# Kernel tuning notes

Measured on AMD Instinct MI355X. Metric: run time of the kernel, lower is better.

## Reference

```python
import jax, jax.numpy as jnp
import numpy as np

N_NODES = 50000
N_EDGES = 800000
F_IN = 128
F_OUT = 128


def setup_inputs() -> dict:
    key = jax.random.key(0)
    k1, k2, k3, k4 = jax.random.split(key, 4)
    x = jax.random.normal(k1, (N_NODES, F_IN), dtype=jnp.float32)
    edge_index = jax.random.randint(k2, (2, N_EDGES), 0, N_NODES, dtype=jnp.int64)
    edge_weight = jax.random.uniform(k3, (N_EDGES,), dtype=jnp.float32)
    # GCNConv linear weight (applied as x @ W) and bias
    W = jax.random.normal(k4, (F_IN, F_OUT), dtype=jnp.float32) / np.sqrt(F_IN)
    b = jnp.zeros((F_OUT,), dtype=jnp.float32)
    return {"x": x, "edge_index": edge_index, "edge_weight": edge_weight, "W": W, "b": b}


def reference(x, edge_index, edge_weight, W, b):
    """Single GCNConv forward (PyG semantics: normalize=True, add_self_loops=True).

    out[i] = sum_{(j->i) in E'} norm_ji * (x[j] @ W) + b
    where E' = E + self loops (weight 1), norm = D^{-1/2} A D^{-1/2}.
    """
    n = x.shape[0]
    # add self loops with weight 1.0
    loops = jnp.arange(n, dtype=edge_index.dtype)
    row = jnp.concatenate([edge_index[0], loops])  # source nodes
    col = jnp.concatenate([edge_index[1], loops])  # target nodes
    ew = jnp.concatenate([edge_weight, jnp.ones((n,), dtype=edge_weight.dtype)])
    # symmetric degree normalization (degree computed at targets, as in PyG gcn_norm)
    deg = jax.ops.segment_sum(ew, col, num_segments=n)
    dinv = jnp.where(deg > 0, jax.lax.rsqrt(deg), 0.0)
    norm = dinv[row] * ew * dinv[col]  # [E+N]
    # linear transform then gather-scale-scatter aggregation
    h = x @ W  # [N, F_OUT]
    msgs = norm[:, None] * h[row]  # [E+N, F_OUT]
    out = jax.ops.segment_sum(msgs, col, num_segments=n) + b
    return out
```

## Files before the change

kernel.cpp:

```cpp
#include <hip/hip_runtime.h>


#define F 128
#define MAXOVF 4096
#define SHIFT 7
#define RNG 128
#define NBMAX 512
#define SA_BS 1024
#define SA_EPB 4096

typedef __attribute__((ext_vector_type(8))) short bf16x8;
typedef __attribute__((ext_vector_type(4))) float f32x4;

__device__ __forceinline__ unsigned bf16rne(float f) {
    unsigned u = __float_as_uint(f);
    return (u + 0x7fffu + ((u >> 16) & 1u)) >> 16;
}
__device__ __forceinline__ float bflo(unsigned u) { return __uint_as_float(u << 16); }
__device__ __forceinline__ float bfhi(unsigned u) { return __uint_as_float(u & 0xffff0000u); }

__global__ __launch_bounds__(1024) void sortA_k(
        const int* __restrict__ row, const int* __restrict__ col,
        const float* __restrict__ ew, const float* __restrict__ x,
        const float* __restrict__ W,
        unsigned* __restrict__ gcnt,
        unsigned long long* __restrict__ stage,
        unsigned* __restrict__ ovf_w, int* __restrict__ ovf, int* __restrict__ ovfc,
        uint4* __restrict__ xb4, unsigned short* __restrict__ Wt,
        int E, int NB, int capb, int SAB, int XB4, long ng8) {
    int tid = threadIdx.x;
    int blk = blockIdx.x;
    if (blk >= SAB) {
        if (blk < SAB + XB4) {
            long i = (long)(blk - SAB) * 1024 + tid;
            if (i < ng8) {
                const float4* x4 = (const float4*)x;
                float4 a = x4[2 * i], c = x4[2 * i + 1];
                uint4 o;
                o.x = bf16rne(a.x) | (bf16rne(a.y) << 16);
                o.y = bf16rne(a.z) | (bf16rne(a.w) << 16);
                o.z = bf16rne(c.x) | (bf16rne(c.y) << 16);
                o.w = bf16rne(c.z) | (bf16rne(c.w) << 16);
                xb4[i] = o;
            }
        } else {
            int idx = (blk - SAB - XB4) * 1024 + tid;
            if (idx < F * F) {
                int k = idx >> 7, nn = idx & 127;
                Wt[nn * F + k] = (unsigned short)bf16rne(W[idx]);
            }
        }
        return;
    }
    __shared__ unsigned hist[NBMAX], sc[NBMAX], rbase[NBMAX], ravail[NBMAX];
    __shared__ unsigned long long stg[SA_EPB];
    unsigned xcc;
    asm volatile("s_getreg_b32 %0, hwreg(HW_REG_XCC_ID, 0, 4)" : "=s"(xcc));
    xcc &= 7u;
    long e0 = (long)blk * SA_EPB;
    for (int i = tid; i < NBMAX; i += SA_BS) hist[i] = 0;
    __syncthreads();
    unsigned long long pk[4];
    int bk[4]; unsigned rk[4];
    #pragma unroll
    for (int k = 0; k < 4; ++k) {
        long e = e0 + k * SA_BS + tid;
        bk[k] = -1;
        if (e < E) {
            int c = col[e], r = row[e];
            float w = ew[e];
            unsigned wq = __float2uint_rn(w * 32768.0f);
            if (wq > 32767u) wq = 32767u;
            pk[k] = ((unsigned long long)(unsigned)c << 32) |
                    ((unsigned long long)(unsigned)r << 15) | wq;
            bk[k] = c >> SHIFT;
            rk[k] = atomicAdd(&hist[bk[k]], 1u);
        }
    }
    __syncthreads();
    if (tid < NBMAX) sc[tid] = hist[tid];
    __syncthreads();
    for (int d = 1; d < NBMAX; d <<= 1) {
        unsigned v = 0;
        if (tid < NBMAX && tid >= d) v = sc[tid - d];
        __syncthreads();
        if (tid < NBMAX) sc[tid] += v;
        __syncthreads();
    }
    if (tid < NB) {
        unsigned cnt = hist[tid], bs = 0, av = 0;
        if (cnt > 0) {
            bs = atomicAdd(&gcnt[xcc * NBMAX + tid], cnt);
            av = (bs < (unsigned)capb) ? ((unsigned)capb - bs) : 0u;
        }
        rbase[tid] = bs;
        ravail[tid] = av;
    }
    __syncthreads();
    #pragma unroll
    for (int k = 0; k < 4; ++k)
        if (bk[k] >= 0) stg[sc[bk[k]] - hist[bk[k]] + rk[k]] = pk[k];
    __syncthreads();
    int tot = (int)sc[NBMAX - 1];
    for (int i = tid; i < tot; i += SA_BS) {
        int lo = 0, hi = NB - 1;
        while (lo < hi) {
            int mid = (lo + hi + 1) >> 1;
            if (sc[mid] - hist[mid] <= (unsigned)i) lo = mid; else hi = mid - 1;
        }
        unsigned j = (unsigned)i - (sc[lo] - hist[lo]);
        unsigned long long v = stg[i];
        if (j < ravail[lo]) {
            stage[((size_t)lo * 8 + xcc) * capb + rbase[lo] + j] = v;
        } else {
            int c = (int)(v >> 32);
            int r = (int)((v >> 15) & 0x1FFFFu);
            unsigned wq = (unsigned)(v & 0x7FFFu);
            atomicAdd(&ovf_w[c], wq);
            int p = atomicAdd(ovfc, 1);
            if (p < MAXOVF) {
                ovf[3 * p] = r; ovf[3 * p + 1] = c; ovf[3 * p + 2] = (int)wq;
            }
        }
    }
}

__global__ __launch_bounds__(1024) void sortB_k(
        const unsigned long long* __restrict__ stage,
        const unsigned* __restrict__ gcnt, const unsigned* __restrict__ ovf_w,
        unsigned* __restrict__ eout, int* __restrict__ offA, int* __restrict__ cntA,
        float* __restrict__ dinv, int n, int capb) {
    __shared__ unsigned cnt[RNG], wsum[RNG], scn[RNG], bex[RNG];
    __shared__ unsigned rpre[9];
    int tid = threadIdx.x;
    int b = blockIdx.x;
    int node0 = b << SHIFT;
    int nodes = n - node0; if (nodes > RNG) nodes = RNG; if (nodes < 0) nodes = 0;
    if (tid < RNG) { cnt[tid] = 0; wsum[tid] = 0; }
    if (tid == 0) {
        unsigned acc = 0; rpre[0] = 0;
        #pragma unroll
        for (int xr = 0; xr < 8; ++xr) {
            unsigned m = gcnt[xr * NBMAX + b]; if (m > (unsigned)capb) m = capb;
            acc += m; rpre[xr + 1] = acc;
        }
    }
    __syncthreads();
    int T = (int)rpre[8];
    unsigned ent[8]; unsigned short noa[8], rka[8];
    int myc = 0;
    for (int i = tid; i < T; i += 1024) {
        int xr = 0;
        while (rpre[xr + 1] <= (unsigned)i) ++xr;
        unsigned j = (unsigned)i - rpre[xr];
        unsigned long long v = stage[((size_t)b * 8 + xr) * capb + j];
        int no = (int)(v >> 32) - node0;
        unsigned wq = (unsigned)(v & 0x7FFFu);
        unsigned rk = atomicAdd(&cnt[no], 1u);
        atomicAdd(&wsum[no], wq);
        ent[myc] = (unsigned)((((v >> 15) & 0x1FFFFu) << 15) | wq);
        noa[myc] = (unsigned short)no; rka[myc] = (unsigned short)rk;
        ++myc;
    }
    __syncthreads();
    if (tid < RNG) scn[tid] = cnt[tid];
    __syncthreads();
    for (int d = 1; d < RNG; d <<= 1) {
        unsigned v = 0;
        if (tid < RNG && tid >= d) v = scn[tid - d];
        __syncthreads();
        if (tid < RNG) scn[tid] += v;
        __syncthreads();
    }
    if (tid < RNG) bex[tid] = scn[tid] - cnt[tid];
    __syncthreads();
    if (tid < nodes) {
        int node = node0 + tid;
        float deg = (float)(wsum[tid] + ovf_w[node]) * (1.0f / 32768.0f) + 1.0f;
        dinv[node] = rsqrtf(deg);
        offA[node] = b * (capb * 8) + (int)bex[tid];
        cntA[node] = (int)cnt[tid];
    }
    unsigned base = (unsigned)(b * (capb * 8));
    for (int k = 0; k < myc; ++k)
        eout[base + bex[noa[k]] + rka[k]] = ent[k];
}

__global__ __launch_bounds__(256) void aggregate_k(
        const uint4* __restrict__ xb4, const float* __restrict__ dinv,
        const int* __restrict__ offA, const int* __restrict__ cntA,
        const unsigned* __restrict__ eout,
        const int* __restrict__ ovf, const int* __restrict__ ovfc,
        uint4* __restrict__ yb4, int n) {
    int lane = threadIdx.x & 63, wv = threadIdx.x >> 6;
    int g = lane >> 4, l = lane & 15;
    int i = blockIdx.x * 16 + wv * 4 + g;
    if (i >= n) return;
    float di = dinv[i];
    uint4 xs = xb4[(size_t)i * 16 + l];
    float a0 = di * bflo(xs.x), a1 = di * bfhi(xs.x);
    float a2 = di * bflo(xs.y), a3 = di * bfhi(xs.y);
    float a4 = di * bflo(xs.z), a5 = di * bfhi(xs.z);
    float a6 = di * bflo(xs.w), a7 = di * bfhi(xs.w);
    int cnt = cntA[i], off = offA[i];
    for (int bb = 0; bb < cnt; bb += 32) {
        int e0 = bb + 2 * l;
        unsigned m0 = (e0     < cnt) ? eout[off + e0]     : 0u;
        unsigned m1 = (e0 + 1 < cnt) ? eout[off + e0 + 1] : 0u;
        int sv0 = (int)(m0 >> 15), sv1 = (int)(m1 >> 15);
        float wk0 = (float)(m0 & 0x7FFFu) * (1.0f / 32768.0f) * dinv[sv0];
        float wk1 = (float)(m1 & 0x7FFFu) * (1.0f / 32768.0f) * dinv[sv1];
        int cb = cnt - bb; if (cb > 32) cb = 32;
        for (int j0 = 0; j0 < cb; j0 += 8) {
            int base = g * 16 + (j0 >> 1);
            int   s0 = __shfl(sv0, base),     s1 = __shfl(sv1, base);
            int   s2 = __shfl(sv0, base + 1), s3 = __shfl(sv1, base + 1);
            int   s4 = __shfl(sv0, base + 2), s5 = __shfl(sv1, base + 2);
            int   s6 = __shfl(sv0, base + 3), s7 = __shfl(sv1, base + 3);
            float w0 = __shfl(wk0, base),     w1 = __shfl(wk1, base);
            float w2 = __shfl(wk0, base + 1), w3 = __shfl(wk1, base + 1);
            float w4 = __shfl(wk0, base + 2), w5 = __shfl(wk1, base + 2);
            float w6 = __shfl(wk0, base + 3), w7 = __shfl(wk1, base + 3);
            uint4 u0 = xb4[(size_t)s0 * 16 + l];
            uint4 u1 = xb4[(size_t)s1 * 16 + l];
            uint4 u2 = xb4[(size_t)s2 * 16 + l];
            uint4 u3 = xb4[(size_t)s3 * 16 + l];
            uint4 u4 = xb4[(size_t)s4 * 16 + l];
            uint4 u5 = xb4[(size_t)s5 * 16 + l];
            uint4 u6 = xb4[(size_t)s6 * 16 + l];
            uint4 u7 = xb4[(size_t)s7 * 16 + l];
            a0 += w0 * bflo(u0.x) + w1 * bflo(u1.x) + w2 * bflo(u2.x) + w3 * bflo(u3.x)
                + w4 * bflo(u4.x) + w5 * bflo(u5.x) + w6 * bflo(u6.x) + w7 * bflo(u7.x);
            a1 += w0 * bfhi(u0.x) + w1 * bfhi(u1.x) + w2 * bfhi(u2.x) + w3 * bfhi(u3.x)
                + w4 * bfhi(u4.x) + w5 * bfhi(u5.x) + w6 * bfhi(u6.x) + w7 * bfhi(u7.x);
            a2 += w0 * bflo(u0.y) + w1 * bflo(u1.y) + w2 * bflo(u2.y) + w3 * bflo(u3.y)
                + w4 * bflo(u4.y) + w5 * bflo(u5.y) + w6 * bflo(u6.y) + w7 * bflo(u7.y);
            a3 += w0 * bfhi(u0.y) + w1 * bfhi(u1.y) + w2 * bfhi(u2.y) + w3 * bfhi(u3.y)
                + w4 * bfhi(u4.y) + w5 * bfhi(u5.y) + w6 * bfhi(u6.y) + w7 * bfhi(u7.y);
            a4 += w0 * bflo(u0.z) + w1 * bflo(u1.z) + w2 * bflo(u2.z) + w3 * bflo(u3.z)
                + w4 * bflo(u4.z) + w5 * bflo(u5.z) + w6 * bflo(u6.z) + w7 * bflo(u7.z);
            a5 += w0 * bfhi(u0.z) + w1 * bfhi(u1.z) + w2 * bfhi(u2.z) + w3 * bfhi(u3.z)
                + w4 * bfhi(u4.z) + w5 * bfhi(u5.z) + w6 * bfhi(u6.z) + w7 * bfhi(u7.z);
            a6 += w0 * bflo(u0.w) + w1 * bflo(u1.w) + w2 * bflo(u2.w) + w3 * bflo(u3.w)
                + w4 * bflo(u4.w) + w5 * bflo(u5.w) + w6 * bflo(u6.w) + w7 * bflo(u7.w);
            a7 += w0 * bfhi(u0.w) + w1 * bfhi(u1.w) + w2 * bfhi(u2.w) + w3 * bfhi(u3.w)
                + w4 * bfhi(u4.w) + w5 * bfhi(u5.w) + w6 * bfhi(u6.w) + w7 * bfhi(u7.w);
        }
    }
    int oc = *ovfc;
    if (oc > 0) {
        if (oc > MAXOVF) oc = MAXOVF;
        for (int k = 0; k < oc; ++k) {
            if (ovf[3 * k + 1] == i) {
                int sv = ovf[3 * k];
                float wk = (float)ovf[3 * k + 2] * (1.0f / 32768.0f) * dinv[sv];
                uint4 u = xb4[(size_t)sv * 16 + l];
                a0 += wk * bflo(u.x); a1 += wk * bfhi(u.x);
                a2 += wk * bflo(u.y); a3 += wk * bfhi(u.y);
                a4 += wk * bflo(u.z); a5 += wk * bfhi(u.z);
                a6 += wk * bflo(u.w); a7 += wk * bfhi(u.w);
            }
        }
    }
    a0 *= di; a1 *= di; a2 *= di; a3 *= di;
    a4 *= di; a5 *= di; a6 *= di; a7 *= di;
    uint4 o;
    o.x = bf16rne(a0) | (bf16rne(a1) << 16);
    o.y = bf16rne(a2) | (bf16rne(a3) << 16);
    o.z = bf16rne(a4) | (bf16rne(a5) << 16);
    o.w = bf16rne(a6) | (bf16rne(a7) << 16);
    yb4[(size_t)i * 16 + l] = o;
}

__global__ __launch_bounds__(256) void gemm_k(const unsigned short* __restrict__ yb,
        const unsigned short* __restrict__ Wt, const float* __restrict__ bias,
        float* __restrict__ out, int n) {
    __shared__ float cs[4][16 * 132];
    int tid = threadIdx.x;
    int w = tid >> 6, lane = tid & 63;
    int m = lane & 15, q = lane >> 4;
    int r0 = blockIdx.x * 64 + w * 16;
    int ar = r0 + m;
    if (ar >= n) ar = n - 1;
    const unsigned short* arow = yb + (size_t)ar * F + q * 8;

    f32x4 acc[8];
    #pragma unroll
    for (int t = 0; t < 8; ++t) acc[t] = (f32x4){0.f, 0.f, 0.f, 0.f};

    #pragma unroll
    for (int kk = 0; kk < 4; ++kk) {
        bf16x8 a = *(const bf16x8*)(arow + kk * 32);
        #pragma unroll
        for (int t = 0; t < 8; ++t) {
            bf16x8 bfr = *(const bf16x8*)(Wt + (size_t)(t * 16 + m) * F + kk * 32 + q * 8);
            acc[t] = __builtin_amdgcn_mfma_f32_16x16x32_bf16(a, bfr, acc[t], 0, 0, 0);
        }
    }

    float* csw = cs[w];
    #pragma unroll
    for (int t = 0; t < 8; ++t)
        #pragma unroll
        for (int v = 0; v < 4; ++v)
            csw[(q * 4 + v) * 132 + t * 16 + m] = acc[t][v];
    int cg = lane & 31;
    float4 bv4 = ((const float4*)bias)[cg];
    #pragma unroll
    for (int rp = 0; rp < 8; ++rp) {
        int rowl = rp * 2 + (lane >> 5);
        int rr = r0 + rowl;
        float4 v4 = *(float4*)&csw[rowl * 132 + cg * 4];
        v4.x += bv4.x; v4.y += bv4.y; v4.z += bv4.z; v4.w += bv4.w;
        if (rr < n) ((float4*)out)[(size_t)rr * 32 + cg] = v4;
    }
}

extern "C" void kernel_launch(void* const* d_in, const int* in_sizes, int n_in,
                              void* d_out, int out_size, void* d_ws, size_t ws_size,
                              hipStream_t stream) {
    const float* x  = (const float*)d_in[0];
    const int*   ei = (const int*)d_in[1];
    const float* ew = (const float*)d_in[2];
    const float* W  = (const float*)d_in[3];
    const float* b  = (const float*)d_in[4];
    float* out = (float*)d_out;

    int n = in_sizes[0] / F;
    int E = in_sizes[2];
    const int* row = ei;
    const int* col = ei + E;
    int NB = (n + RNG - 1) >> SHIFT;

    float* ws = (float*)d_ws;
    size_t o = 0;
    auto take = [&](size_t elems) { size_t r = o; o += (elems + 63) & ~63ull; return r; };
    size_t o_gcnt  = take(8 * NBMAX);
    size_t o_ovfc  = take(64);
    size_t o_ovfw  = take(n);
    size_t zero_end = o;
    size_t o_ovf   = take((size_t)MAXOVF * 3);
    size_t o_dinv  = take(n);
    size_t o_offA  = take(n);
    size_t o_cntA  = take(n);
    size_t o_wt    = take(F * F / 2);
    size_t o_xb    = take((size_t)n * (F / 2));
    size_t o_yb    = take((size_t)n * (F / 2));
    size_t units = ws_size / 4;
    size_t remain = (units > o + 128) ? (units - o - 128) : 0;
    int capb = (int)(remain / ((size_t)NB * 8 * 3));
    if (capb > 1024) capb = 1024;
    if (capb < 256)  capb = 256;
    size_t o_stage = take((size_t)NB * 8 * capb * 2);
    size_t o_eout  = take((size_t)NB * 8 * capb);
    (void)n_in; (void)out_size; (void)o_eout;

    unsigned* gcnt = (unsigned*)(ws + o_gcnt);
    int*      ovfc = (int*)(ws + o_ovfc);
    unsigned* ovfw = (unsigned*)(ws + o_ovfw);
    int*      ovf  = (int*)(ws + o_ovf);
    float*    dinv = ws + o_dinv;
    int*      offA = (int*)(ws + o_offA);
    int*      cntA = (int*)(ws + o_cntA);
    unsigned short* Wt = (unsigned short*)(ws + o_wt);
    unsigned* xb   = (unsigned*)(ws + o_xb);
    unsigned* yb   = (unsigned*)(ws + o_yb);
    unsigned long long* stage = (unsigned long long*)(ws + o_stage);
    unsigned* eout = (unsigned*)(ws + o_eout);

    hipMemsetAsync(d_ws, 0, zero_end * sizeof(float), stream);

    int SAB = (E + SA_EPB - 1) / SA_EPB;
    long ng8 = (long)n * (F / 8);
    int XB4 = (int)((ng8 + 1023) / 1024);
    int WB = (F * F + 1023) / 1024;

    sortA_k<<<SAB + XB4 + WB, SA_BS, 0, stream>>>(row, col, ew, x, W, gcnt, stage,
                                                  ovfw, ovf, ovfc, (uint4*)xb, Wt,
                                                  E, NB, capb, SAB, XB4, ng8);
    sortB_k<<<NB, SA_BS, 0, stream>>>(stage, gcnt, ovfw, eout, offA, cntA,
                                      dinv, n, capb);
    aggregate_k<<<(n + 15) / 16, 256, 0, stream>>>((const uint4*)xb, dinv, offA,
                                                   cntA, eout, ovf, ovfc,
                                                   (uint4*)yb, n);
    gemm_k<<<(n + 63) / 64, 256, 0, stream>>>((const unsigned short*)yb, Wt, b, out, n);
}
```

Before: 150.9 us.

## Fuse aggregation with bf16 MFMA GEMM and cache bucket ids in sort

Aggregation and the projection GEMM are merged into one kernel. Each 512-thread block aggregates 32 nodes into shared memory, then runs MFMA against the transposed weights and writes the output with bias added. This removes the bf16 intermediate buffer's global write and read plus one kernel launch. Separately, the sort pass stores each staged entry's bucket id in shared memory, replacing a per-element binary search over the prefix sums. In exchange, the extra shared memory and the launch-bounds hint may lower occupancy during the gather-heavy aggregation phase.

```diff
diff --git a/kernel.cpp b/kernel.cpp
--- a/kernel.cpp
+++ b/kernel.cpp
@@ -54,6 +54,7 @@
     }
     __shared__ unsigned hist[NBMAX], sc[NBMAX], rbase[NBMAX], ravail[NBMAX];
     __shared__ unsigned long long stg[SA_EPB];
+    __shared__ unsigned short bkid[SA_EPB];
     unsigned xcc;
     asm volatile("s_getreg_b32 %0, hwreg(HW_REG_XCC_ID, 0, 4)" : "=s"(xcc));
     xcc &= 7u;
@@ -99,15 +100,15 @@
     __syncthreads();
     #pragma unroll
     for (int k = 0; k < 4; ++k)
-        if (bk[k] >= 0) stg[sc[bk[k]] - hist[bk[k]] + rk[k]] = pk[k];
+        if (bk[k] >= 0) {
+            unsigned slot = sc[bk[k]] - hist[bk[k]] + rk[k];
+            stg[slot] = pk[k];
+            bkid[slot] = (unsigned short)bk[k];
+        }
     __syncthreads();
     int tot = (int)sc[NBMAX - 1];
     for (int i = tid; i < tot; i += SA_BS) {
-        int lo = 0, hi = NB - 1;
-        while (lo < hi) {
-            int mid = (lo + hi + 1) >> 1;
-            if (sc[mid] - hist[mid] <= (unsigned)i) lo = mid; else hi = mid - 1;
-        }
+        int lo = (int)bkid[i];
         unsigned j = (unsigned)i - (sc[lo] - hist[lo]);
         unsigned long long v = stg[i];
         if (j < ravail[lo]) {
@@ -186,133 +187,131 @@
         eout[base + bex[noa[k]] + rka[k]] = ent[k];
 }
 
-__global__ __launch_bounds__(256) void aggregate_k(
+__global__ __launch_bounds__(512, 6) void agg_gemm_k(
         const uint4* __restrict__ xb4, const float* __restrict__ dinv,
         const int* __restrict__ offA, const int* __restrict__ cntA,
         const unsigned* __restrict__ eout,
         const int* __restrict__ ovf, const int* __restrict__ ovfc,
-        uint4* __restrict__ yb4, int n) {
-    int lane = threadIdx.x & 63, wv = threadIdx.x >> 6;
-    int g = lane >> 4, l = lane & 15;
-    int i = blockIdx.x * 16 + wv * 4 + g;
-    if (i >= n) return;
-    float di = dinv[i];
-    uint4 xs = xb4[(size_t)i * 16 + l];
-    float a0 = di * bflo(xs.x), a1 = di * bfhi(xs.x);
-    float a2 = di * bflo(xs.y), a3 = di * bfhi(xs.y);
-    float a4 = di * bflo(xs.z), a5 = di * bfhi(xs.z);
-    float a6 = di * bflo(xs.w), a7 = di * bfhi(xs.w);
-    int cnt = cntA[i], off = offA[i];
-    for (int bb = 0; bb < cnt; bb += 32) {
-        int e0 = bb + 2 * l;
-        unsigned m0 = (e0     < cnt) ? eout[off + e0]     : 0u;
-        unsigned m1 = (e0 + 1 < cnt) ? eout[off + e0 + 1] : 0u;
-        int sv0 = (int)(m0 >> 15), sv1 = (int)(m1 >> 15);
-        float wk0 = (float)(m0 & 0x7FFFu) * (1.0f / 32768.0f) * dinv[sv0];
-        float wk1 = (float)(m1 & 0x7FFFu) * (1.0f / 32768.0f) * dinv[sv1];
-        int cb = cnt - bb; if (cb > 32) cb = 32;
-        for (int j0 = 0; j0 < cb; j0 += 8) {
-            int base = g * 16 + (j0 >> 1);
-            int   s0 = __shfl(sv0, base),     s1 = __shfl(sv1, base);
-            int   s2 = __shfl(sv0, base + 1), s3 = __shfl(sv1, base + 1);
-            int   s4 = __shfl(sv0, base + 2), s5 = __shfl(sv1, base + 2);
-            int   s6 = __shfl(sv0, base + 3), s7 = __shfl(sv1, base + 3);
-            float w0 = __shfl(wk0, base),     w1 = __shfl(wk1, base);
-            float w2 = __shfl(wk0, base + 1), w3 = __shfl(wk1, base + 1);
-            float w4 = __shfl(wk0, base + 2), w5 = __shfl(wk1, base + 2);
-            float w6 = __shfl(wk0, base + 3), w7 = __shfl(wk1, base + 3);
-            uint4 u0 = xb4[(size_t)s0 * 16 + l];
-            uint4 u1 = xb4[(size_t)s1 * 16 + l];
-            uint4 u2 = xb4[(size_t)s2 * 16 + l];
-            uint4 u3 = xb4[(size_t)s3 * 16 + l];
-            uint4 u4 = xb4[(size_t)s4 * 16 + l];
-            uint4 u5 = xb4[(size_t)s5 * 16 + l];
-            uint4 u6 = xb4[(size_t)s6 * 16 + l];
-            uint4 u7 = xb4[(size_t)s7 * 16 + l];
-            a0 += w0 * bflo(u0.x) + w1 * bflo(u1.x) + w2 * bflo(u2.x) + w3 * bflo(u3.x)
-                + w4 * bflo(u4.x) + w5 * bflo(u5.x) + w6 * bflo(u6.x) + w7 * bflo(u7.x);
-            a1 += w0 * bfhi(u0.x) + w1 * bfhi(u1.x) + w2 * bfhi(u2.x) + w3 * bfhi(u3.x)
-                + w4 * bfhi(u4.x) + w5 * bfhi(u5.x) + w6 * bfhi(u6.x) + w7 * bfhi(u7.x);
-            a2 += w0 * bflo(u0.y) + w1 * bflo(u1.y) + w2 * bflo(u2.y) + w3 * bflo(u3.y)
-                + w4 * bflo(u4.y) + w5 * bflo(u5.y) + w6 * bflo(u6.y) + w7 * bflo(u7.y);
-            a3 += w0 * bfhi(u0.y) + w1 * bfhi(u1.y) + w2 * bfhi(u2.y) + w3 * bfhi(u3.y)
-                + w4 * bfhi(u4.y) + w5 * bfhi(u5.y) + w6 * bfhi(u6.y) + w7 * bfhi(u7.y);
-            a4 += w0 * bflo(u0.z) + w1 * bflo(u1.z) + w2 * bflo(u2.z) + w3 * bflo(u3.z)
-                + w4 * bflo(u4.z) + w5 * bflo(u5.z) + w6 * bflo(u6.z) + w7 * bflo(u7.z);
-            a5 += w0 * bfhi(u0.z) + w1 * bfhi(u1.z) + w2 * bfhi(u2.z) + w3 * bfhi(u3.z)
-                + w4 * bfhi(u4.z) + w5 * bfhi(u5.z) + w6 * bfhi(u6.z) + w7 * bfhi(u7.z);
-            a6 += w0 * bflo(u0.w) + w1 * bflo(u1.w) + w2 * bflo(u2.w) + w3 * bflo(u3.w)
-                + w4 * bflo(u4.w) + w5 * bflo(u5.w) + w6 * bflo(u6.w) + w7 * bflo(u7.w);
-            a7 += w0 * bfhi(u0.w) + w1 * bfhi(u1.w) + w2 * bfhi(u2.w) + w3 * bfhi(u3.w)
-                + w4 * bfhi(u4.w) + w5 * bfhi(u5.w) + w6 * bfhi(u6.w) + w7 * bfhi(u7.w);
-        }
-    }
-    int oc = *ovfc;
-    if (oc > 0) {
-        if (oc > MAXOVF) oc = MAXOVF;
-        for (int k = 0; k < oc; ++k) {
-            if (ovf[3 * k + 1] == i) {
-                int sv = ovf[3 * k];
-                float wk = (float)ovf[3 * k + 2] * (1.0f / 32768.0f) * dinv[sv];
-                uint4 u = xb4[(size_t)sv * 16 + l];
-                a0 += wk * bflo(u.x); a1 += wk * bfhi(u.x);
-                a2 += wk * bflo(u.y); a3 += wk * bfhi(u.y);
-                a4 += wk * bflo(u.z); a5 += wk * bfhi(u.z);
-                a6 += wk * bflo(u.w); a7 += wk * bfhi(u.w);
-            }
-        }
-    }
-    a0 *= di; a1 *= di; a2 *= di; a3 *= di;
-    a4 *= di; a5 *= di; a6 *= di; a7 *= di;
-    uint4 o;
-    o.x = bf16rne(a0) | (bf16rne(a1) << 16);
-    o.y = bf16rne(a2) | (bf16rne(a3) << 16);
-    o.z = bf16rne(a4) | (bf16rne(a5) << 16);
-    o.w = bf16rne(a6) | (bf16rne(a7) << 16);
-    yb4[(size_t)i * 16 + l] = o;
-}
-
-__global__ __launch_bounds__(256) void gemm_k(const unsigned short* __restrict__ yb,
         const unsigned short* __restrict__ Wt, const float* __restrict__ bias,
         float* __restrict__ out, int n) {
-    __shared__ float cs[4][16 * 132];
-    int tid = threadIdx.x;
-    int w = tid >> 6, lane = tid & 63;
-    int m = lane & 15, q = lane >> 4;
-    int r0 = blockIdx.x * 64 + w * 16;
-    int ar = r0 + m;
-    if (ar >= n) ar = n - 1;
-    const unsigned short* arow = yb + (size_t)ar * F + q * 8;
-
-    f32x4 acc[8];
-    #pragma unroll
-    for (int t = 0; t < 8; ++t) acc[t] = (f32x4){0.f, 0.f, 0.f, 0.f};
-
-    #pragma unroll
-    for (int kk = 0; kk < 4; ++kk) {
-        bf16x8 a = *(const bf16x8*)(arow + kk * 32);
+    __shared__ unsigned ys[32 * 68];
+    __shared__ float epi[8][2 * 320];
+    int wv = threadIdx.x >> 6, lane = threadIdx.x & 63;
+
+    {
+        int g = lane >> 4, l = lane & 15;
+        int nl = wv * 4 + g;
+        int i = blockIdx.x * 32 + nl;
+        if (i < n) {
+            float di = dinv[i];
+            uint4 xs = xb4[(size_t)i * 16 + l];
+            float a0 = di * bflo(xs.x), a1 = di * bfhi(xs.x);
+            float a2 = di * bflo(xs.y), a3 = di * bfhi(xs.y);
+            float a4 = di * bflo(xs.z), a5 = di * bfhi(xs.z);
+            float a6 = di * bflo(xs.w), a7 = di * bfhi(xs.w);
+            int cnt = cntA[i], off = offA[i];
+            for (int bb = 0; bb < cnt; bb += 32) {
+                int e0 = bb + 2 * l;
+                unsigned m0 = (e0     < cnt) ? eout[off + e0]     : 0u;
+                unsigned m1 = (e0 + 1 < cnt) ? eout[off + e0 + 1] : 0u;
+                int sv0 = (int)(m0 >> 15), sv1 = (int)(m1 >> 15);
+                float wk0 = (float)(m0 & 0x7FFFu) * (1.0f / 32768.0f) * dinv[sv0];
+                float wk1 = (float)(m1 & 0x7FFFu) * (1.0f / 32768.0f) * dinv[sv1];
+                int cb = cnt - bb; if (cb > 32) cb = 32;
+                for (int j0 = 0; j0 < cb; j0 += 8) {
+                    int base = g * 16 + (j0 >> 1);
+                    int   s0 = __shfl(sv0, base),     s1 = __shfl(sv1, base);
+                    int   s2 = __shfl(sv0, base + 1), s3 = __shfl(sv1, base + 1);
+                    int   s4 = __shfl(sv0, base + 2), s5 = __shfl(sv1, base + 2);
+                    int   s6 = __shfl(sv0, base + 3), s7 = __shfl(sv1, base + 3);
+                    float w0 = __shfl(wk0, base),     w1 = __shfl(wk1, base);
+                    float w2 = __shfl(wk0, base + 1), w3 = __shfl(wk1, base + 1);
+                    float w4 = __shfl(wk0, base + 2), w5 = __shfl(wk1, base + 2);
+                    float w6 = __shfl(wk0, base + 3), w7 = __shfl(wk1, base + 3);
+                    uint4 u0 = xb4[(size_t)s0 * 16 + l];
+                    uint4 u1 = xb4[(size_t)s1 * 16 + l];
+                    uint4 u2 = xb4[(size_t)s2 * 16 + l];
+                    uint4 u3 = xb4[(size_t)s3 * 16 + l];
+                    uint4 u4 = xb4[(size_t)s4 * 16 + l];
+                    uint4 u5 = xb4[(size_t)s5 * 16 + l];
+                    uint4 u6 = xb4[(size_t)s6 * 16 + l];
+                    uint4 u7 = xb4[(size_t)s7 * 16 + l];
+                    a0 += w0 * bflo(u0.x) + w1 * bflo(u1.x) + w2 * bflo(u2.x) + w3 * bflo(u3.x)
+                        + w4 * bflo(u4.x) + w5 * bflo(u5.x) + w6 * bflo(u6.x) + w7 * bflo(u7.x);
+                    a1 += w0 * bfhi(u0.x) + w1 * bfhi(u1.x) + w2 * bfhi(u2.x) + w3 * bfhi(u3.x)
+                        + w4 * bfhi(u4.x) + w5 * bfhi(u5.x) + w6 * bfhi(u6.x) + w7 * bfhi(u7.x);
+                    a2 += w0 * bflo(u0.y) + w1 * bflo(u1.y) + w2 * bflo(u2.y) + w3 * bflo(u3.y)
+                        + w4 * bflo(u4.y) + w5 * bflo(u5.y) + w6 * bflo(u6.y) + w7 * bflo(u7.y);
+                    a3 += w0 * bfhi(u0.y) + w1 * bfhi(u1.y) + w2 * bfhi(u2.y) + w3 * bfhi(u3.y)
+                        + w4 * bfhi(u4.y) + w5 * bfhi(u5.y) + w6 * bfhi(u6.y) + w7 * bfhi(u7.y);
+                    a4 += w0 * bflo(u0.z) + w1 * bflo(u1.z) + w2 * bflo(u2.z) + w3 * bflo(u3.z)
+                        + w4 * bflo(u4.z) + w5 * bflo(u5.z) + w6 * bflo(u6.z) + w7 * bflo(u7.z);
+                    a5 += w0 * bfhi(u0.z) + w1 * bfhi(u1.z) + w2 * bfhi(u2.z) + w3 * bfhi(u3.z)
+                        + w4 * bfhi(u4.z) + w5 * bfhi(u5.z) + w6 * bfhi(u6.z) + w7 * bfhi(u7.z);
+                    a6 += w0 * bflo(u0.w) + w1 * bflo(u1.w) + w2 * bflo(u2.w) + w3 * bflo(u3.w)
+                        + w4 * bflo(u4.w) + w5 * bflo(u5.w) + w6 * bflo(u6.w) + w7 * bflo(u7.w);
+                    a7 += w0 * bfhi(u0.w) + w1 * bfhi(u1.w) + w2 * bfhi(u2.w) + w3 * bfhi(u3.w)
+                        + w4 * bfhi(u4.w) + w5 * bfhi(u5.w) + w6 * bfhi(u6.w) + w7 * bfhi(u7.w);
+                }
+            }
+            int oc = *ovfc;
+            if (oc > 0) {
+                if (oc > MAXOVF) oc = MAXOVF;
+                for (int k = 0; k < oc; ++k) {
+                    if (ovf[3 * k + 1] == i) {
+                        int sv = ovf[3 * k];
+                        float wk = (float)ovf[3 * k + 2] * (1.0f / 32768.0f) * dinv[sv];
+                        uint4 u = xb4[(size_t)sv * 16 + l];
+                        a0 += wk * bflo(u.x); a1 += wk * bfhi(u.x);
+                        a2 += wk * bflo(u.y); a3 += wk * bfhi(u.y);
+                        a4 += wk * bflo(u.z); a5 += wk * bfhi(u.z);
+                        a6 += wk * bflo(u.w); a7 += wk * bfhi(u.w);
+                    }
+                }
+            }
+            a0 *= di; a1 *= di; a2 *= di; a3 *= di;
+            a4 *= di; a5 *= di; a6 *= di; a7 *= di;
+            uint4 o;
+            o.x = bf16rne(a0) | (bf16rne(a1) << 16);
+            o.y = bf16rne(a2) | (bf16rne(a3) << 16);
+            o.z = bf16rne(a4) | (bf16rne(a5) << 16);
+            o.w = bf16rne(a6) | (bf16rne(a7) << 16);
+            *(uint4*)&ys[nl * 68 + l * 4] = o;
+        }
+    }
+    __syncthreads();
+
+    {
+        int m = lane & 15, q = lane >> 4;
+        int rt = wv & 1;
+        int ct0 = wv >> 1;
+        int gr0 = blockIdx.x * 32 + rt * 16;
+        f32x4 acc0 = (f32x4){0.f, 0.f, 0.f, 0.f};
+        f32x4 acc1 = (f32x4){0.f, 0.f, 0.f, 0.f};
         #pragma unroll
-        for (int t = 0; t < 8; ++t) {
-            bf16x8 bfr = *(const bf16x8*)(Wt + (size_t)(t * 16 + m) * F + kk * 32 + q * 8);
-            acc[t] = __builtin_amdgcn_mfma_f32_16x16x32_bf16(a, bfr, acc[t], 0, 0, 0);
-        }
-    }
-
-    float* csw = cs[w];
-    #pragma unroll
-    for (int t = 0; t < 8; ++t)
+        for (int kk = 0; kk < 4; ++kk) {
+            bf16x8 a = *(const bf16x8*)&ys[(rt * 16 + m) * 68 + kk * 16 + q * 4];
+            bf16x8 b0 = *(const bf16x8*)(Wt + (size_t)(ct0 * 16 + m) * F + kk * 32 + q * 8);
+            bf16x8 b1 = *(const bf16x8*)(Wt + (size_t)((ct0 + 4) * 16 + m) * F + kk * 32 + q * 8);
+            acc0 = __builtin_amdgcn_mfma_f32_16x16x32_bf16(a, b0, acc0, 0, 0, 0);
+            acc1 = __builtin_amdgcn_mfma_f32_16x16x32_bf16(a, b1, acc1, 0, 0, 0);
+        }
+        float* ep = epi[wv];
         #pragma unroll
-        for (int v = 0; v < 4; ++v)
-            csw[(q * 4 + v) * 132 + t * 16 + m] = acc[t][v];
-    int cg = lane & 31;
-    float4 bv4 = ((const float4*)bias)[cg];
-    #pragma unroll
-    for (int rp = 0; rp < 8; ++rp) {
-        int rowl = rp * 2 + (lane >> 5);
-        int rr = r0 + rowl;
-        float4 v4 = *(float4*)&csw[rowl * 132 + cg * 4];
-        v4.x += bv4.x; v4.y += bv4.y; v4.z += bv4.z; v4.w += bv4.w;
-        if (rr < n) ((float4*)out)[(size_t)rr * 32 + cg] = v4;
+        for (int v = 0; v < 4; ++v) {
+            ep[(q * 4 + v) * 20 + m]       = acc0[v];
+            ep[320 + (q * 4 + v) * 20 + m] = acc1[v];
+        }
+        int r = lane >> 2, c4 = lane & 3;
+        #pragma unroll
+        for (int tt = 0; tt < 2; ++tt) {
+            int ct = ct0 + tt * 4;
+            float4 bv = ((const float4*)bias)[ct * 4 + c4];
+            float4 v4 = *(float4*)&ep[tt * 320 + r * 20 + c4 * 4];
+            v4.x += bv.x; v4.y += bv.y; v4.z += bv.z; v4.w += bv.w;
+            int rr = gr0 + r;
+            if (rr < n) ((float4*)out)[(size_t)rr * 32 + ct * 4 + c4] = v4;
+        }
     }
 }
 
@@ -345,7 +344,6 @@
     size_t o_cntA  = take(n);
     size_t o_wt    = take(F * F / 2);
     size_t o_xb    = take((size_t)n * (F / 2));
-    size_t o_yb    = take((size_t)n * (F / 2));
     size_t units = ws_size / 4;
     size_t remain = (units > o + 128) ? (units - o - 128) : 0;
     int capb = (int)(remain / ((size_t)NB * 8 * 3));
@@ -364,7 +362,6 @@
     int*      cntA = (int*)(ws + o_cntA);
     unsigned short* Wt = (unsigned short*)(ws + o_wt);
     unsigned* xb   = (unsigned*)(ws + o_xb);
-    unsigned* yb   = (unsigned*)(ws + o_yb);
     unsigned long long* stage = (unsigned long long*)(ws + o_stage);
     unsigned* eout = (unsigned*)(ws + o_eout);
 
@@ -380,8 +377,7 @@
                                                   E, NB, capb, SAB, XB4, ng8);
     sortB_k<<<NB, SA_BS, 0, stream>>>(stage, gcnt, ovfw, eout, offA, cntA,
                                       dinv, n, capb);
-    aggregate_k<<<(n + 15) / 16, 256, 0, stream>>>((const uint4*)xb, dinv, offA,
-                                                   cntA, eout, ovf, ovfc,
-                                                   (uint4*)yb, n);
-    gemm_k<<<(n + 63) / 64, 256, 0, stream>>>((const unsigned short*)yb, Wt, b, out, n);
-}
+    agg_gemm_k<<<(n + 31) / 32, 512, 0, stream>>>((const uint4*)xb, dinv, offA,
+                                                  cntA, eout, ovf, ovfc, Wt, b,
+                                                  out, n);
+}
```

New measurement: 141.8 us. 6.1% less time.
